# Performance work log

Hardware: AMD Instinct MI355X
Metric: run time of the kernel (lower is better)

Reference implementation:

```python
import jax, jax.numpy as jnp
import numpy as np

EPS = 1e-6
START, END, FACTOR = 2.0, 8.0, 0.5


def layer_norm(x, w, b):
    mu = jnp.mean(x, axis=-1, keepdims=True)
    var = jnp.mean(jnp.square(x - mu), axis=-1, keepdims=True)
    return (x - mu) * jax.lax.rsqrt(var + EPS) * w + b


def build_spread_vector(hsize):
    # decay_i = factor ** (1 / k_i), k_i linearly spaced in [start, end]
    return FACTOR ** (1.0 / jnp.linspace(START, END, hsize, dtype=jnp.float32))


def decay_scan(decay, u):
    # cx[t] = decay * cx[t-1] + u[t], along axis 1 (seq). decay: [H], u: [B,S,H]
    a = jnp.broadcast_to(decay, u.shape)

    def combine(c1, c2):
        a1, b1 = c1
        a2, b2 = c2
        return a1 * a2, a2 * b1 + b2

    _, cx = jax.lax.associative_scan(combine, (a, u), axis=1)
    return cx


def setup_inputs() -> dict:
    key = jax.random.key(0)
    ks = jax.random.split(key, 4)
    B, S, D = 8, 2048, 1024
    sd = 1.0 / np.sqrt(D)
    return {
        "x": jax.random.normal(ks[0], (B, S, D), jnp.float32),
        "Wt": jax.random.normal(ks[1], (D, D), jnp.float32) * sd,
        "Wo": jax.random.normal(ks[2], (D, D), jnp.float32) * sd,
        "Wg": jax.random.normal(ks[3], (2 * D, D), jnp.float32) * sd,
        "bg": jnp.zeros((D,), jnp.float32),
        "ln1_w": jnp.ones((D,), jnp.float32),
        "ln1_b": jnp.zeros((D,), jnp.float32),
        "lnc_w": jnp.ones((D,), jnp.float32),
        "lnc_b": jnp.zeros((D,), jnp.float32),
        "lng_w": jnp.ones((D,), jnp.float32),
        "lng_b": jnp.zeros((D,), jnp.float32),
    }


def reference(x, Wt, Wo, Wg, bg, ln1_w, ln1_b, lnc_w, lnc_b, lng_w, lng_b):
    H = Wt.shape[1]
    decay = build_spread_vector(H)            # [H]
    decay_beta = 1.0 - decay
    _x = layer_norm(x, ln1_w, ln1_b)          # [B,S,D]
    u = jnp.einsum("bsd,dh->bsh", _x, Wt) * decay_beta
    cx = decay_scan(decay, u)                 # [B,S,H]
    out = jnp.einsum("bsh,hd->bsd", layer_norm(cx, lnc_w, lnc_b), Wo)
    res = _x                                  # norm_residual=True
    gate = jax.nn.sigmoid(
        layer_norm(jnp.concatenate((res, out), axis=-1) @ Wg + bg, lng_w, lng_b)
    )
    return (1.0 - gate) * res + gate * out
```

## Files before the change

### kernel.cpp

```cpp
#include <hip/hip_runtime.h>
#include <hip/hip_bf16.h>
#include <cmath>
#include <cstdint>

namespace {

constexpr int kB = 8;
constexpr int kS = 2048;
constexpr int kD = 1024;
constexpr int kN = kB * kS;
constexpr int kChunk = 128;
constexpr int kNChunk = kS / kChunk;
constexpr float kEps = 1e-6f;

typedef __attribute__((ext_vector_type(8))) short bf16x8;
typedef __attribute__((ext_vector_type(4))) float f32x4;

__device__ inline float bf2f(short s) {
  union { unsigned u; float f; } c;
  c.u = ((unsigned)(unsigned short)s) << 16;
  return c.f;
}

struct bh4 { __hip_bfloat16 a, b, c, d; };

__device__ inline void gload16(const void* g, void* l) {
  __builtin_amdgcn_global_load_lds(
      (const __attribute__((address_space(1))) void*)g,
      (__attribute__((address_space(3))) void*)l, 16, 0, 0);
}

__device__ inline void blockReduce2(float& s1, float& s2) {
#pragma unroll
  for (int off = 32; off > 0; off >>= 1) {
    s1 += __shfl_down(s1, off);
    s2 += __shfl_down(s2, off);
  }
  __shared__ float r1[4], r2[4];
  int wid = threadIdx.x >> 6;
  if ((threadIdx.x & 63) == 0) { r1[wid] = s1; r2[wid] = s2; }
  __syncthreads();
  s1 = r1[0] + r1[1] + r1[2] + r1[3];
  s2 = r2[0] + r2[1] + r2[2] + r2[3];
}

__global__ __launch_bounds__(256) void k_prep(
    const float* __restrict__ Wt, const float* __restrict__ Wo,
    const float* __restrict__ Wg, __hip_bfloat16* __restrict__ WtT,
    __hip_bfloat16* __restrict__ WoT, __hip_bfloat16* __restrict__ WgT,
    float* __restrict__ decay, float* __restrict__ dbeta,
    float* __restrict__ aL) {
  int b = blockIdx.x;
  int t = threadIdx.x;
  if (b < 4) {
    int h = b * 256 + t;
    float kk = 2.0f + 6.0f * (float)h / (float)(kD - 1);
    float d = exp2f(-1.0f / kk);
    decay[h] = d;
    dbeta[h] = 1.0f - d;
    aL[h] = exp2f(-(float)kChunk / kk);
    return;
  }
  b -= 4;
  const float* W;
  __hip_bfloat16* WT;
  int K, local;
  if (b < 1024)      { W = Wt; WT = WtT; K = kD;     local = b; }
  else if (b < 2048) { W = Wo; WT = WoT; K = kD;     local = b - 1024; }
  else               { W = Wg; WT = WgT; K = 2 * kD; local = b - 2048; }
  int n0 = (local & 31) * 32, k0 = (local >> 5) * 32;
  __shared__ float tile[32][33];
  int tr = t >> 3, tc4 = (t & 7) * 4;
  float4 v = *reinterpret_cast<const float4*>(W + (size_t)(k0 + tr) * kD + n0 + tc4);
  tile[tc4 + 0][tr] = v.x;
  tile[tc4 + 1][tr] = v.y;
  tile[tc4 + 2][tr] = v.z;
  tile[tc4 + 3][tr] = v.w;
  __syncthreads();
  bh4 o;
  o.a = __float2bfloat16(tile[tr][tc4 + 0]);
  o.b = __float2bfloat16(tile[tr][tc4 + 1]);
  o.c = __float2bfloat16(tile[tr][tc4 + 2]);
  o.d = __float2bfloat16(tile[tr][tc4 + 3]);
  *reinterpret_cast<bh4*>(WT + (size_t)(n0 + tr) * K + k0 + tc4) = o;
}

__global__ __launch_bounds__(256) void k_ln_f32in(
    const float* __restrict__ x, const float* __restrict__ w,
    const float* __restrict__ b, __hip_bfloat16* __restrict__ y) {
  int row = blockIdx.x;
  int t = threadIdx.x;
  const float4 v = reinterpret_cast<const float4*>(x + (size_t)row * kD)[t];
  float s1 = v.x + v.y + v.z + v.w;
  float s2 = v.x * v.x + v.y * v.y + v.z * v.z + v.w * v.w;
  blockReduce2(s1, s2);
  float mu = s1 * (1.0f / kD);
  float var = s2 * (1.0f / kD) - mu * mu;
  float rs = rsqrtf(var + kEps);
  float4 wv = reinterpret_cast<const float4*>(w)[t];
  float4 bv = reinterpret_cast<const float4*>(b)[t];
  bh4 o;
  o.a = __float2bfloat16((v.x - mu) * rs * wv.x + bv.x);
  o.b = __float2bfloat16((v.y - mu) * rs * wv.y + bv.y);
  o.c = __float2bfloat16((v.z - mu) * rs * wv.z + bv.z);
  o.d = __float2bfloat16((v.w - mu) * rs * wv.w + bv.w);
  reinterpret_cast<bh4*>(y + (size_t)row * kD)[t] = o;
}

__global__ __launch_bounds__(256) void k_ln_bf16in(
    const __hip_bfloat16* __restrict__ x, const float* __restrict__ w,
    const float* __restrict__ b, __hip_bfloat16* __restrict__ y) {
  int row = blockIdx.x;
  int t = threadIdx.x;
  short4 q = reinterpret_cast<const short4*>(x + (size_t)row * kD)[t];
  float vv[4] = {bf2f(q.x), bf2f(q.y), bf2f(q.z), bf2f(q.w)};
  float s1 = vv[0] + vv[1] + vv[2] + vv[3];
  float s2 = vv[0] * vv[0] + vv[1] * vv[1] + vv[2] * vv[2] + vv[3] * vv[3];
  blockReduce2(s1, s2);
  float mu = s1 * (1.0f / kD);
  float var = s2 * (1.0f / kD) - mu * mu;
  float rs = rsqrtf(var + kEps);
  float4 wv = reinterpret_cast<const float4*>(w)[t];
  float4 bv = reinterpret_cast<const float4*>(b)[t];
  bh4 o;
  o.a = __float2bfloat16((vv[0] - mu) * rs * wv.x + bv.x);
  o.b = __float2bfloat16((vv[1] - mu) * rs * wv.y + bv.y);
  o.c = __float2bfloat16((vv[2] - mu) * rs * wv.z + bv.z);
  o.d = __float2bfloat16((vv[3] - mu) * rs * wv.w + bv.w);
  reinterpret_cast<bh4*>(y + (size_t)row * kD)[t] = o;
}

__global__ __launch_bounds__(512, 2) void k_mfma_gemm(
    const __hip_bfloat16* __restrict__ A1, const __hip_bfloat16* __restrict__ A2,
    const __hip_bfloat16* __restrict__ BT, int K,
    float* __restrict__ C, __hip_bfloat16* __restrict__ Cb,
    const float* __restrict__ colscale, const float* __restrict__ bias) {
  __shared__ short As[2][2][8192];
  __shared__ short Bs[2][2][8192];
  const int t = threadIdx.x;
  const int wid = t >> 6, lane = t & 63;
  const int nwg = gridDim.x;
  const int bid = blockIdx.x;
  const int s = (bid & 7) * (nwg >> 3) + (bid >> 3);
  const int bn = (s & 3) * 256;
  const int bm = (s >> 2) * 256;
  const int wr = wid >> 2;
  const int wcn = wid & 3;
  const int r = lane & 15, kg = lane >> 4;
  const int NT = K / 64;

  const int srow = lane >> 3;
  const int scol = (((lane & 7) ^ srow)) * 8;

  auto stageA = [&](int kt, int h) {
    const __hip_bfloat16* Asrc = A1;
    int kk = kt * 64;
    if (A2 && kk >= kD) { Asrc = A2; kk -= kD; }
    short* dst = &As[kt & 1][h][0];
#pragma unroll
    for (int j = 0; j < 2; ++j) {
      int chunk = wid * 2 + j;
      int row = chunk * 8 + srow;
      gload16(Asrc + (size_t)(bm + h * 128 + row) * kD + kk + scol,
              dst + chunk * 512 + lane * 8);
    }
  };
  auto stageB = [&](int kt, int h) {
    short* dst = &Bs[kt & 1][h][0];
#pragma unroll
    for (int j = 0; j < 2; ++j) {
      int chunk = wid * 2 + j;
      int row = chunk * 8 + srow;
      gload16(BT + (size_t)(bn + h * 128 + row) * K + kt * 64 + scol,
              dst + chunk * 512 + lane * 8);
    }
  };

  f32x4 acc[8][4];
#pragma unroll
  for (int m = 0; m < 8; ++m)
#pragma unroll
    for (int n = 0; n < 4; ++n) acc[m][n] = (f32x4){0.f, 0.f, 0.f, 0.f};

  stageA(0, 0); stageA(0, 1); stageB(0, 0); stageB(0, 1);
  stageB(1, 0); stageB(1, 1);
  asm volatile("s_waitcnt vmcnt(4)" ::: "memory");
  __builtin_amdgcn_s_barrier();
  asm volatile("" ::: "memory");

  for (int T = 0; T < NT; ++T) {
    const int bc = T & 1;
    const char* Ab = reinterpret_cast<const char*>(&As[bc][wr][0]);
    const char* Bb = reinterpret_cast<const char*>(&Bs[bc][wcn >> 1][0]);
    const int bcol = (wcn & 1) * 64;
    bf16x8 bfr[4][2], aLO[4][2], aHI[4][2];
#pragma unroll
    for (int n = 0; n < 4; ++n)
#pragma unroll
      for (int ks = 0; ks < 2; ++ks) {
        int row = bcol + n * 16 + r;
        int slot = (ks * 4 + kg) ^ (r & 7);
        bfr[n][ks] = *reinterpret_cast<const bf16x8*>(Bb + row * 128 + slot * 16);
      }
#pragma unroll
    for (int mm = 0; mm < 4; ++mm)
#pragma unroll
      for (int ks = 0; ks < 2; ++ks) {
        int row = mm * 16 + r;
        int slot = (ks * 4 + kg) ^ (r & 7);
        aLO[mm][ks] = *reinterpret_cast<const bf16x8*>(Ab + row * 128 + slot * 16);
      }
    if (T + 1 < NT) { stageA(T + 1, 0); stageA(T + 1, 1); }
    asm volatile("" ::: "memory");
    __builtin_amdgcn_s_barrier();
    asm volatile("" ::: "memory");
    __builtin_amdgcn_s_setprio(1);
#pragma unroll
    for (int mm = 0; mm < 4; ++mm)
#pragma unroll
      for (int n = 0; n < 4; ++n)
#pragma unroll
        for (int ks = 0; ks < 2; ++ks)
          acc[mm][n] = __builtin_amdgcn_mfma_f32_16x16x32_bf16(
              aLO[mm][ks], bfr[n][ks], acc[mm][n], 0, 0, 0);
    __builtin_amdgcn_s_setprio(0);
    asm volatile("" ::: "memory");
    __builtin_amdgcn_s_barrier();
    asm volatile("" ::: "memory");
#pragma unroll
    for (int mm = 0; mm < 4; ++mm)
#pragma unroll
      for (int ks = 0; ks < 2; ++ks) {
        int row = (mm + 4) * 16 + r;
        int slot = (ks * 4 + kg) ^ (r & 7);
        aHI[mm][ks] = *reinterpret_cast<const bf16x8*>(Ab + row * 128 + slot * 16);
      }
    if (T + 2 < NT) { stageB(T + 2, 0); stageB(T + 2, 1); }
    asm volatile("" ::: "memory");
    __builtin_amdgcn_s_barrier();
    asm volatile("" ::: "memory");
    __builtin_amdgcn_s_setprio(1);
#pragma unroll
    for (int mm = 0; mm < 4; ++mm)
#pragma unroll
      for (int n = 0; n < 4; ++n)
#pragma unroll
        for (int ks = 0; ks < 2; ++ks)
          acc[mm + 4][n] = __builtin_amdgcn_mfma_f32_16x16x32_bf16(
              aHI[mm][ks], bfr[n][ks], acc[mm + 4][n], 0, 0, 0);
    __builtin_amdgcn_s_setprio(0);
    if (T + 2 < NT)
      asm volatile("s_waitcnt vmcnt(4)" ::: "memory");
    else if (T + 1 < NT)
      asm volatile("s_waitcnt vmcnt(0)" ::: "memory");
    asm volatile("" ::: "memory");
    __builtin_amdgcn_s_barrier();
    asm volatile("" ::: "memory");
  }

  int col[4];
  float cs[4], bi[4];
#pragma unroll
  for (int n = 0; n < 4; ++n) {
    col[n] = bn + wcn * 64 + n * 16 + r;
    cs[n] = colscale ? colscale[col[n]] : 1.0f;
    bi[n] = bias ? bias[col[n]] : 0.0f;
  }
#pragma unroll
  for (int m = 0; m < 8; ++m) {
#pragma unroll
    for (int j = 0; j < 4; ++j) {
      int row = bm + wr * 128 + m * 16 + kg * 4 + j;
#pragma unroll
      for (int n = 0; n < 4; ++n) {
        float v = acc[m][n][j] * cs[n] + bi[n];
        if (C) C[(size_t)row * kD + col[n]] = v;
        if (Cb) Cb[(size_t)row * kD + col[n]] = __float2bfloat16(v);
      }
    }
  }
}

__global__ __launch_bounds__(256) void k_scan_ends(
    const __hip_bfloat16* __restrict__ u, const float* __restrict__ decay,
    float* __restrict__ ends) {
  int tid = blockIdx.x * blockDim.x + threadIdx.x;
  int h = tid & (kD - 1);
  int c = (tid >> 10) & (kNChunk - 1);
  int b = tid >> 14;
  float a = decay[h];
  const __hip_bfloat16* up =
      u + ((size_t)(b * kS) + (size_t)c * kChunk) * kD + h;
  float v = 0.f;
#pragma unroll 8
  for (int i = 0; i < kChunk; ++i)
    v = fmaf(a, v, bf2f(*(const short*)(up + (size_t)i * kD)));
  ends[tid] = v;
}

__global__ __launch_bounds__(256) void k_scan_carry(
    const float* __restrict__ ends, const float* __restrict__ aL,
    float* __restrict__ carry) {
  int tid = blockIdx.x * blockDim.x + threadIdx.x;
  int h = tid & (kD - 1);
  int b = tid >> 10;
  float al = aL[h];
  float car = 0.f;
#pragma unroll
  for (int c = 0; c < kNChunk; ++c) {
    size_t idx = ((size_t)(b * kNChunk + c)) * kD + h;
    carry[idx] = car;
    car = fmaf(al, car, ends[idx]);
  }
}

__global__ __launch_bounds__(256) void k_scan_apply(
    __hip_bfloat16* __restrict__ u, const float* __restrict__ decay,
    const float* __restrict__ carry) {
  int tid = blockIdx.x * blockDim.x + threadIdx.x;
  int h = tid & (kD - 1);
  int c = (tid >> 10) & (kNChunk - 1);
  int b = tid >> 14;
  float a = decay[h];
  float v = carry[tid];
  __hip_bfloat16* up = u + ((size_t)(b * kS) + (size_t)c * kChunk) * kD + h;
#pragma unroll 8
  for (int i = 0; i < kChunk; ++i) {
    v = fmaf(a, v, bf2f(*(const short*)(up + (size_t)i * kD)));
    up[(size_t)i * kD] = __float2bfloat16(v);
  }
}

__global__ __launch_bounds__(256) void k_final(
    const __hip_bfloat16* __restrict__ gpre, const __hip_bfloat16* __restrict__ res,
    const __hip_bfloat16* __restrict__ outp, const float* __restrict__ w,
    const float* __restrict__ b, float* __restrict__ y) {
  int row = blockIdx.x;
  int t = threadIdx.x;
  short4 q = reinterpret_cast<const short4*>(gpre + (size_t)row * kD)[t];
  float vv[4] = {bf2f(q.x), bf2f(q.y), bf2f(q.z), bf2f(q.w)};
  float s1 = vv[0] + vv[1] + vv[2] + vv[3];
  float s2 = vv[0] * vv[0] + vv[1] * vv[1] + vv[2] * vv[2] + vv[3] * vv[3];
  blockReduce2(s1, s2);
  float mu = s1 * (1.0f / kD);
  float var = s2 * (1.0f / kD) - mu * mu;
  float rs = rsqrtf(var + kEps);
  float4 wv = reinterpret_cast<const float4*>(w)[t];
  float4 bv = reinterpret_cast<const float4*>(b)[t];
  short4 r4 = reinterpret_cast<const short4*>(res + (size_t)row * kD)[t];
  short4 o4 = reinterpret_cast<const short4*>(outp + (size_t)row * kD)[t];
  float rr[4] = {bf2f(r4.x), bf2f(r4.y), bf2f(r4.z), bf2f(r4.w)};
  float oo[4] = {bf2f(o4.x), bf2f(o4.y), bf2f(o4.z), bf2f(o4.w)};
  float ww[4] = {wv.x, wv.y, wv.z, wv.w};
  float bb[4] = {bv.x, bv.y, bv.z, bv.w};
  float4 out;
  float* op = &out.x;
#pragma unroll
  for (int i = 0; i < 4; ++i) {
    float z = (vv[i] - mu) * rs * ww[i] + bb[i];
    float g = 1.0f / (1.0f + expf(-z));
    op[i] = rr[i] + g * (oo[i] - rr[i]);
  }
  reinterpret_cast<float4*>(y + (size_t)row * kD)[t] = out;
}

}

extern "C" void kernel_launch(void* const* d_in, const int* in_sizes, int n_in,
                              void* d_out, int out_size, void* d_ws,
                              size_t ws_size, hipStream_t stream) {
  const float* x = (const float*)d_in[0];
  const float* Wt = (const float*)d_in[1];
  const float* Wo = (const float*)d_in[2];
  const float* Wg = (const float*)d_in[3];
  const float* bg = (const float*)d_in[4];
  const float* ln1w = (const float*)d_in[5];
  const float* ln1b = (const float*)d_in[6];
  const float* lncw = (const float*)d_in[7];
  const float* lncb = (const float*)d_in[8];
  const float* lngw = (const float*)d_in[9];
  const float* lngb = (const float*)d_in[10];
  float* y = (float*)d_out;

  char* ws = (char*)d_ws;
  size_t off = 0;
  auto alloc = [&](size_t bytes) {
    char* p = ws + off;
    off += (bytes + 255) & ~(size_t)255;
    return p;
  };
  __hip_bfloat16* xnb = (__hip_bfloat16*)alloc((size_t)kN * kD * 2);
  __hip_bfloat16* ub = (__hip_bfloat16*)alloc((size_t)kN * kD * 2);
  __hip_bfloat16* outb = (__hip_bfloat16*)alloc((size_t)kN * kD * 2);
  __hip_bfloat16* cxn = (__hip_bfloat16*)alloc((size_t)kN * kD * 2);
  __hip_bfloat16* WtT = (__hip_bfloat16*)alloc((size_t)kD * kD * 2);
  __hip_bfloat16* WoT = (__hip_bfloat16*)alloc((size_t)kD * kD * 2);
  __hip_bfloat16* WgT = (__hip_bfloat16*)alloc((size_t)kD * 2 * kD * 2);
  float* decay = (float*)alloc(kD * 4);
  float* dbeta = (float*)alloc(kD * 4);
  float* aL = (float*)alloc(kD * 4);
  float* ends = (float*)alloc((size_t)kB * kNChunk * kD * 4);
  float* carry = (float*)alloc((size_t)kB * kNChunk * kD * 4);

  const int nwg = (kD / 256) * (kN / 256);

  k_prep<<<4 + 1024 + 1024 + 2048, 256, 0, stream>>>(
      Wt, Wo, Wg, WtT, WoT, WgT, decay, dbeta, aL);
  k_ln_f32in<<<kN, 256, 0, stream>>>(x, ln1w, ln1b, xnb);
  k_mfma_gemm<<<nwg, 512, 0, stream>>>(xnb, nullptr, WtT, kD, nullptr, ub,
                                       dbeta, nullptr);
  k_scan_ends<<<(kB * kNChunk * kD) / 256, 256, 0, stream>>>(ub, decay, ends);
  k_scan_carry<<<(kB * kD) / 256, 256, 0, stream>>>(ends, aL, carry);
  k_scan_apply<<<(kB * kNChunk * kD) / 256, 256, 0, stream>>>(ub, decay, carry);
  k_ln_bf16in<<<kN, 256, 0, stream>>>(ub, lncw, lncb, cxn);
  k_mfma_gemm<<<nwg, 512, 0, stream>>>(cxn, nullptr, WoT, kD, nullptr, outb,
                                       nullptr, nullptr);
  k_mfma_gemm<<<nwg, 512, 0, stream>>>(xnb, outb, WgT, 2 * kD, nullptr, ub,
                                       nullptr, bg);
  k_final<<<kN, 256, 0, stream>>>(ub, xnb, outb, lngw, lngb, y);
}
```

Baseline: 231.9 us.

## Fuse chunk-end scan into GEMM epilogue and merge layernorm into prep kernel

```diff
diff --git a/kernel.cpp b/kernel.cpp
--- a/kernel.cpp
+++ b/kernel.cpp
@@ -44,7 +44,9 @@
   s2 = r2[0] + r2[1] + r2[2] + r2[3];
 }
 
-__global__ __launch_bounds__(256) void k_prep(
+__global__ __launch_bounds__(256) void k_prep_ln(
+    const float* __restrict__ x, const float* __restrict__ ln1w,
+    const float* __restrict__ ln1b, __hip_bfloat16* __restrict__ xnb,
     const float* __restrict__ Wt, const float* __restrict__ Wo,
     const float* __restrict__ Wg, __hip_bfloat16* __restrict__ WtT,
     __hip_bfloat16* __restrict__ WoT, __hip_bfloat16* __restrict__ WgT,
@@ -52,6 +54,26 @@
     float* __restrict__ aL) {
   int b = blockIdx.x;
   int t = threadIdx.x;
+  if (b < kN) {
+    int row = b;
+    const float4 v = reinterpret_cast<const float4*>(x + (size_t)row * kD)[t];
+    float s1 = v.x + v.y + v.z + v.w;
+    float s2 = v.x * v.x + v.y * v.y + v.z * v.z + v.w * v.w;
+    blockReduce2(s1, s2);
+    float mu = s1 * (1.0f / kD);
+    float var = s2 * (1.0f / kD) - mu * mu;
+    float rs = rsqrtf(var + kEps);
+    float4 wv = reinterpret_cast<const float4*>(ln1w)[t];
+    float4 bv = reinterpret_cast<const float4*>(ln1b)[t];
+    bh4 o;
+    o.a = __float2bfloat16((v.x - mu) * rs * wv.x + bv.x);
+    o.b = __float2bfloat16((v.y - mu) * rs * wv.y + bv.y);
+    o.c = __float2bfloat16((v.z - mu) * rs * wv.z + bv.z);
+    o.d = __float2bfloat16((v.w - mu) * rs * wv.w + bv.w);
+    reinterpret_cast<bh4*>(xnb + (size_t)row * kD)[t] = o;
+    return;
+  }
+  b -= kN;
   if (b < 4) {
     int h = b * 256 + t;
     float kk = 2.0f + 6.0f * (float)h / (float)(kD - 1);
@@ -85,28 +107,6 @@
   *reinterpret_cast<bh4*>(WT + (size_t)(n0 + tr) * K + k0 + tc4) = o;
 }
 
-__global__ __launch_bounds__(256) void k_ln_f32in(
-    const float* __restrict__ x, const float* __restrict__ w,
-    const float* __restrict__ b, __hip_bfloat16* __restrict__ y) {
-  int row = blockIdx.x;
-  int t = threadIdx.x;
-  const float4 v = reinterpret_cast<const float4*>(x + (size_t)row * kD)[t];
-  float s1 = v.x + v.y + v.z + v.w;
-  float s2 = v.x * v.x + v.y * v.y + v.z * v.z + v.w * v.w;
-  blockReduce2(s1, s2);
-  float mu = s1 * (1.0f / kD);
-  float var = s2 * (1.0f / kD) - mu * mu;
-  float rs = rsqrtf(var + kEps);
-  float4 wv = reinterpret_cast<const float4*>(w)[t];
-  float4 bv = reinterpret_cast<const float4*>(b)[t];
-  bh4 o;
-  o.a = __float2bfloat16((v.x - mu) * rs * wv.x + bv.x);
-  o.b = __float2bfloat16((v.y - mu) * rs * wv.y + bv.y);
-  o.c = __float2bfloat16((v.z - mu) * rs * wv.z + bv.z);
-  o.d = __float2bfloat16((v.w - mu) * rs * wv.w + bv.w);
-  reinterpret_cast<bh4*>(y + (size_t)row * kD)[t] = o;
-}
-
 __global__ __launch_bounds__(256) void k_ln_bf16in(
     const __hip_bfloat16* __restrict__ x, const float* __restrict__ w,
     const float* __restrict__ b, __hip_bfloat16* __restrict__ y) {
@@ -134,7 +134,8 @@
     const __hip_bfloat16* __restrict__ A1, const __hip_bfloat16* __restrict__ A2,
     const __hip_bfloat16* __restrict__ BT, int K,
     float* __restrict__ C, __hip_bfloat16* __restrict__ Cb,
-    const float* __restrict__ colscale, const float* __restrict__ bias) {
+    const float* __restrict__ colscale, const float* __restrict__ bias,
+    float* __restrict__ ends, const float* __restrict__ decay) {
   __shared__ short As[2][2][8192];
   __shared__ short Bs[2][2][8192];
   const int t = threadIdx.x;
@@ -279,23 +280,37 @@
       }
     }
   }
-}
-
-__global__ __launch_bounds__(256) void k_scan_ends(
-    const __hip_bfloat16* __restrict__ u, const float* __restrict__ decay,
-    float* __restrict__ ends) {
-  int tid = blockIdx.x * blockDim.x + threadIdx.x;
-  int h = tid & (kD - 1);
-  int c = (tid >> 10) & (kNChunk - 1);
-  int b = tid >> 14;
-  float a = decay[h];
-  const __hip_bfloat16* up =
-      u + ((size_t)(b * kS) + (size_t)c * kChunk) * kD + h;
-  float v = 0.f;
-#pragma unroll 8
-  for (int i = 0; i < kChunk; ++i)
-    v = fmaf(a, v, bf2f(*(const short*)(up + (size_t)i * kD)));
-  ends[tid] = v;
+
+  if (ends) {
+    const int row0 = bm + wr * 128;
+    const int eidx = (row0 >> 7) * kD;
+#pragma unroll
+    for (int n = 0; n < 4; ++n) {
+      float a = decay[col[n]];
+      float a2 = a * a, a4 = a2 * a2, a8 = a4 * a4, a16 = a8 * a8;
+      float pw = (kg == 3) ? 1.0f
+               : (kg == 2) ? a4
+               : (kg == 1) ? a4 * a4
+                           : a4 * a4 * a4;
+      float w[4];
+      w[3] = pw;
+      w[2] = pw * a;
+      w[1] = pw * a2;
+      w[0] = pw * a2 * a;
+      float p = 0.f;
+#pragma unroll
+      for (int m = 7; m >= 0; --m) {
+#pragma unroll
+        for (int j = 0; j < 4; ++j)
+          p += w[j] * (acc[m][n][j] * cs[n] + bi[n]);
+#pragma unroll
+        for (int j = 0; j < 4; ++j) w[j] *= a16;
+      }
+      p += __shfl_xor(p, 16);
+      p += __shfl_xor(p, 32);
+      if (kg == 0) ends[eidx + col[n]] = p;
+    }
+  }
 }
 
 __global__ __launch_bounds__(256) void k_scan_carry(
@@ -404,18 +419,16 @@
 
   const int nwg = (kD / 256) * (kN / 256);
 
-  k_prep<<<4 + 1024 + 1024 + 2048, 256, 0, stream>>>(
-      Wt, Wo, Wg, WtT, WoT, WgT, decay, dbeta, aL);
-  k_ln_f32in<<<kN, 256, 0, stream>>>(x, ln1w, ln1b, xnb);
+  k_prep_ln<<<kN + 4 + 4096, 256, 0, stream>>>(
+      x, ln1w, ln1b, xnb, Wt, Wo, Wg, WtT, WoT, WgT, decay, dbeta, aL);
   k_mfma_gemm<<<nwg, 512, 0, stream>>>(xnb, nullptr, WtT, kD, nullptr, ub,
-                                       dbeta, nullptr);
-  k_scan_ends<<<(kB * kNChunk * kD) / 256, 256, 0, stream>>>(ub, decay, ends);
+                                       dbeta, nullptr, ends, decay);
   k_scan_carry<<<(kB * kD) / 256, 256, 0, stream>>>(ends, aL, carry);
   k_scan_apply<<<(kB * kNChunk * kD) / 256, 256, 0, stream>>>(ub, decay, carry);
   k_ln_bf16in<<<kN, 256, 0, stream>>>(ub, lncw, lncb, cxn);
   k_mfma_gemm<<<nwg, 512, 0, stream>>>(cxn, nullptr, WoT, kD, nullptr, outb,
-                                       nullptr, nullptr);
+                                       nullptr, nullptr, nullptr, nullptr);
   k_mfma_gemm<<<nwg, 512, 0, stream>>>(xnb, outb, WgT, 2 * kD, nullptr, ub,
-                                       nullptr, bg);
+                                       nullptr, bg, nullptr, nullptr);
   k_final<<<kN, 256, 0, stream>>>(ub, xnb, outb, lngw, lngb, y);
 }
```

New measurement: 222.7 us. -4.0%, faster.
